# Kernel tuning notes

Hardware: AMD Instinct MI355X
Metric: run time of the kernel (lower is better)

The kernel has to match this reference:

```python
import jax, jax.numpy as jnp
import numpy as np

N_LAYERS = 4
D_MODEL = 256
N_HEADS = 8
D_FF = 2 * D_MODEL
EPS_ATTN = 1e-6
EPS_LN = 1e-5


def setup_inputs() -> dict:
    key = jax.random.key(0)
    ks = jax.random.split(key, 20)
    C, F, L = D_MODEL, D_FF, N_LAYERS
    s = 0.02
    return {
        "ref_feature": jax.random.normal(ks[0], (4, C, 128, 128), jnp.float32),
        # per-layer stacked params (torch nn.Linear convention: y = x @ W.T + b)
        "Wq": jax.random.normal(ks[1], (L, C, C), jnp.float32) * s,
        "bq": jnp.zeros((L, C), jnp.float32),
        "Wk": jax.random.normal(ks[2], (L, C, C), jnp.float32) * s,
        "bk": jnp.zeros((L, C), jnp.float32),
        "Wv": jax.random.normal(ks[3], (L, C, C), jnp.float32) * s,
        "bv": jnp.zeros((L, C), jnp.float32),
        "Wo": jax.random.normal(ks[4], (L, C, C), jnp.float32) * s,
        "bo": jnp.zeros((L, C), jnp.float32),
        "g1": jnp.ones((L, C), jnp.float32),
        "be1": jnp.zeros((L, C), jnp.float32),
        "W1": jax.random.normal(ks[5], (L, F, C), jnp.float32) * s,
        "c1": jnp.zeros((L, F), jnp.float32),
        "W2": jax.random.normal(ks[6], (L, C, F), jnp.float32) * s,
        "c2": jnp.zeros((L, C), jnp.float32),
        "g2": jnp.ones((L, C), jnp.float32),
        "be2": jnp.zeros((L, C), jnp.float32),
    }


def _layer_norm(x, g, b):
    m = jnp.mean(x, axis=-1, keepdims=True)
    v = jnp.mean(jnp.square(x - m), axis=-1, keepdims=True)
    return (x - m) * jax.lax.rsqrt(v + EPS_LN) * g + b


def _feature_map(x):
    return jax.nn.elu(x) + 1.0


def reference(ref_feature, Wq, bq, Wk, bk, Wv, bv, Wo, bo,
              g1, be1, W1, c1, W2, c2, g2, be2):
    N, C, H, W = ref_feature.shape
    Hh, D = N_HEADS, C // N_HEADS
    # patch embed: flatten to tokens [N, HW, C]
    x = ref_feature.reshape(N, C, H * W).transpose(0, 2, 1)

    def body(x, p):
        (Wq_, bq_, Wk_, bk_, Wv_, bv_, Wo_, bo_,
         g1_, be1_, W1_, c1_, W2_, c2_, g2_, be2_) = p
        L = x.shape[1]
        q = (x @ Wq_.T + bq_).reshape(N, L, Hh, D)
        k = (x @ Wk_.T + bk_).reshape(N, L, Hh, D)
        v = (x @ Wv_.T + bv_).reshape(N, L, Hh, D)
        Q = _feature_map(q)
        K = _feature_map(k)
        KV = jnp.einsum('nshd,nshm->nhmd', K, v)            # [N,H,D,D]
        Z = 1.0 / (jnp.einsum('nlhd,nhd->nlh', Q, K.sum(axis=1)) + EPS_ATTN)
        attn = jnp.einsum('nlhd,nhmd,nlh->nlhm', Q, KV, Z).reshape(N, L, C)
        x = _layer_norm(x + attn @ Wo_.T + bo_, g1_, be1_)
        y = jax.nn.relu(x @ W1_.T + c1_) @ W2_.T + c2_
        x = _layer_norm(x + y, g2_, be2_)
        return x, x

    params = (Wq, bq, Wk, bk, Wv, bv, Wo, bo,
              g1, be1, W1, c1, W2, c2, g2, be2)
    _, ys = jax.lax.scan(body, x, params)
    # ys: [n_layers, N, HW, C] -> [n_layers, N, C, H, W]
    return ys.transpose(0, 1, 3, 2).reshape(N_LAYERS, N, C, H, W)
```

## Files before the change

### kernel.cpp

```cpp
#include <hip/hip_runtime.h>
#include <hip/hip_bf16.h>
#include <math.h>

#define NB     4
#define CDIM   256
#define HWDIM  16384
#define LTOK   16384
#define NH     8
#define HD     32
#define FF     512
#define MTOK   (NB * LTOK)
#define NLAYER 4

typedef __bf16 bf16x8 __attribute__((ext_vector_type(8)));
typedef __bf16 bf16x4 __attribute__((ext_vector_type(4)));
typedef float  floatx4 __attribute__((ext_vector_type(4)));

#define GLD16(gp, lp)                                                        \
    __builtin_amdgcn_global_load_lds(                                        \
        (const __attribute__((address_space(1))) void*)(gp),                 \
        (__attribute__((address_space(3))) void*)(lp), 16, 0, 0)

__global__ __launch_bounds__(256)
void f2b_kernel(const float* __restrict__ in, __bf16* __restrict__ out)
{
    int i = (blockIdx.x * 256 + threadIdx.x) * 4;
    float4 f = *(const float4*)&in[i];
    bf16x4 h;
    h[0] = (__bf16)f.x; h[1] = (__bf16)f.y; h[2] = (__bf16)f.z; h[3] = (__bf16)f.w;
    *(bf16x4*)&out[i] = h;
}

__global__ __launch_bounds__(256)
void patch_embed(const float* __restrict__ in, __bf16* __restrict__ out)
{
    __shared__ float tile[32][33];
    const int n = blockIdx.z;
    const int hw0 = blockIdx.x * 32, c0 = blockIdx.y * 32;
    const int tx = threadIdx.x, ty = threadIdx.y;
#pragma unroll
    for (int i = 0; i < 32; i += 8)
        tile[ty + i][tx] = in[(long long)n * CDIM * HWDIM + (long long)(c0 + ty + i) * HWDIM + hw0 + tx];
    __syncthreads();
#pragma unroll
    for (int i = 0; i < 32; i += 8)
        out[(long long)(n * HWDIM + hw0 + ty + i) * CDIM + c0 + tx] = (__bf16)tile[tx][ty + i];
}

__global__ __launch_bounds__(256)
void out_transpose(const __bf16* __restrict__ X, float* __restrict__ out)
{
    __shared__ float tile[32][33];
    const int n = blockIdx.z;
    const int c0 = blockIdx.x * 32, l0 = blockIdx.y * 32;
    const int tid = threadIdx.x;
    {
        int row = tid >> 3, cq = tid & 7;
        bf16x4 x4 = *(const bf16x4*)&X[(long long)(n * LTOK + l0 + row) * CDIM + c0 + cq * 4];
#pragma unroll
        for (int j = 0; j < 4; ++j)
            tile[row][cq * 4 + j] = (float)x4[j];
    }
    __syncthreads();
    {
        int r = tid >> 3, lg = tid & 7;
        float4 o;
        o.x = tile[lg * 4 + 0][r];
        o.y = tile[lg * 4 + 1][r];
        o.z = tile[lg * 4 + 2][r];
        o.w = tile[lg * 4 + 3][r];
        *(float4*)&out[(long long)n * CDIM * LTOK + (long long)(c0 + r) * LTOK + l0 + lg * 4] = o;
    }
}

#define WIDE_PROLOGUE()                                                      \
    const int tid  = threadIdx.x;                                            \
    const int lane = tid & 63;                                               \
    const int wave = tid >> 6;                                               \
    const int m0   = blockIdx.x * 128;                                       \
    const int l15  = lane & 15;                                              \
    const int quad = lane >> 4;                                              \
    const int wm   = (wave & 1) * 64;                                        \
    const int wn   = (wave >> 1) * 128;                                      \
    floatx4 acc[4][8];                                                       \
    _Pragma("unroll")                                                        \
    for (int i = 0; i < 4; ++i)                                              \
        _Pragma("unroll")                                                    \
        for (int j = 0; j < 8; ++j)                                          \
            acc[i][j] = (floatx4){0.f, 0.f, 0.f, 0.f};

#define WIDE_STAGE(Aq, Bq, KD)                                               \
    __syncthreads();                                                         \
    _Pragma("unroll")                                                        \
    for (int i = 0; i < 4; ++i) {                                            \
        int s = wave * 256 + i * 64 + lane;                                  \
        int row = s >> 3, kq = s & 7;                                        \
        GLD16(&(Aq)[(long long)(m0 + row) * (KD) + k0 + kq * 8],             \
              &Asl[(wave * 256 + i * 64) * 8]);                              \
    }                                                                        \
    _Pragma("unroll")                                                        \
    for (int i = 0; i < 8; ++i) {                                            \
        int s = wave * 512 + i * 64 + lane;                                  \
        int row = s >> 3, kq = s & 7;                                        \
        GLD16(&(Bq)[(long long)row * (KD) + k0 + kq * 8],                    \
              &Bsl[(wave * 512 + i * 64) * 8]);                              \
    }                                                                        \
    __syncthreads();

#define WIDE_MFMA()                                                          \
    _Pragma("unroll")                                                        \
    for (int ko = 0; ko < 2; ++ko) {                                         \
        bf16x8 af[4], bfr[8];                                                \
        _Pragma("unroll")                                                    \
        for (int mt = 0; mt < 4; ++mt)                                       \
            af[mt] = *(const bf16x8*)&Asl[(wm + mt * 16 + l15) * 64 + ko * 32 + quad * 8]; \
        _Pragma("unroll")                                                    \
        for (int nt = 0; nt < 8; ++nt)                                       \
            bfr[nt] = *(const bf16x8*)&Bsl[(wn + nt * 16 + l15) * 64 + ko * 32 + quad * 8]; \
        _Pragma("unroll")                                                    \
        for (int mt = 0; mt < 4; ++mt)                                       \
            _Pragma("unroll")                                                \
            for (int nt = 0; nt < 8; ++nt)                                   \
                acc[mt][nt] = __builtin_amdgcn_mfma_f32_16x16x32_bf16(       \
                    bfr[nt], af[mt], acc[mt][nt], 0, 0, 0);                  \
    }

__global__ __launch_bounds__(256, 2)
void gemm_qkv(const __bf16* __restrict__ X,
              const __bf16* __restrict__ Wq, const __bf16* __restrict__ Wk,
              const __bf16* __restrict__ Wv,
              const float* __restrict__ bq, const float* __restrict__ bk,
              const float* __restrict__ bv,
              __bf16* __restrict__ Qo, __bf16* __restrict__ Ko,
              __bf16* __restrict__ Vo)
{
    __shared__ __bf16 Asl[128 * 64];
    __shared__ __bf16 Bsl[256 * 64];
    const int sel = blockIdx.y;
    const __bf16* B    = (sel == 0) ? Wq : (sel == 1) ? Wk : Wv;
    const float*  bias = (sel == 0) ? bq : (sel == 1) ? bk : bv;
    __bf16*       C    = (sel == 0) ? Qo : (sel == 1) ? Ko : Vo;
    const bool do_elu  = sel < 2;

    WIDE_PROLOGUE()
    for (int k0 = 0; k0 < CDIM; k0 += 64) {
        WIDE_STAGE(X, B, CDIM)
        WIDE_MFMA()
    }
#pragma unroll
    for (int mt = 0; mt < 4; ++mt) {
        int row = m0 + wm + mt * 16 + l15;
#pragma unroll
        for (int nt = 0; nt < 8; ++nt) {
            int col0 = wn + nt * 16 + quad * 4;
            float4 bb = *(const float4*)&bias[col0];
            bf16x4 o;
#pragma unroll
            for (int r = 0; r < 4; ++r) {
                float v = acc[mt][nt][r] + ((r == 0) ? bb.x : (r == 1) ? bb.y : (r == 2) ? bb.z : bb.w);
                if (do_elu) v = v > 0.f ? v + 1.f : __expf(v);
                o[r] = (__bf16)v;
            }
            *(bf16x4*)&C[(long long)row * CDIM + col0] = o;
        }
    }
}

__global__ __launch_bounds__(256, 2)
void gemm_relu(const __bf16* __restrict__ A, const __bf16* __restrict__ Bw,
               const float* __restrict__ bias, __bf16* __restrict__ C)
{
    __shared__ __bf16 Asl[128 * 64];
    __shared__ __bf16 Bsl[256 * 64];
    const int n_base = blockIdx.y * 256;
    const __bf16* B = Bw + (long long)n_base * CDIM;

    WIDE_PROLOGUE()
    for (int k0 = 0; k0 < CDIM; k0 += 64) {
        WIDE_STAGE(A, B, CDIM)
        WIDE_MFMA()
    }
#pragma unroll
    for (int mt = 0; mt < 4; ++mt) {
        int row = m0 + wm + mt * 16 + l15;
#pragma unroll
        for (int nt = 0; nt < 8; ++nt) {
            int col0 = wn + nt * 16 + quad * 4;
            float4 bb = *(const float4*)&bias[n_base + col0];
            bf16x4 o;
#pragma unroll
            for (int r = 0; r < 4; ++r) {
                float v = acc[mt][nt][r] + ((r == 0) ? bb.x : (r == 1) ? bb.y : (r == 2) ? bb.z : bb.w);
                o[r] = (__bf16)(v > 0.f ? v : 0.f);
            }
            *(bf16x4*)&C[(long long)row * FF + n_base + col0] = o;
        }
    }
}

template <int KDIM>
__global__ __launch_bounds__(256, 2)
void gemm_ln(const __bf16* __restrict__ A, const __bf16* __restrict__ B,
             const float* __restrict__ bias, __bf16* X,
             const float* __restrict__ g, const float* __restrict__ be)
{
    __shared__ __bf16 Asl[128 * 64];
    __shared__ __bf16 Bsl[256 * 64];

    WIDE_PROLOGUE()
    for (int k0 = 0; k0 < KDIM; k0 += 64) {
        WIDE_STAGE(A, B, KDIM)
        WIDE_MFMA()
    }

#pragma unroll
    for (int mt = 0; mt < 4; ++mt) {
        int row = m0 + wm + mt * 16 + l15;
#pragma unroll
        for (int nt = 0; nt < 8; ++nt) {
            int col0 = wn + nt * 16 + quad * 4;
            float4 bb = *(const float4*)&bias[col0];
            bf16x4 xr = *(const bf16x4*)&X[(long long)row * CDIM + col0];
            acc[mt][nt][0] += bb.x + (float)xr[0];
            acc[mt][nt][1] += bb.y + (float)xr[1];
            acc[mt][nt][2] += bb.z + (float)xr[2];
            acc[mt][nt][3] += bb.w + (float)xr[3];
        }
    }

    float psum[4], psq[4];
#pragma unroll
    for (int mt = 0; mt < 4; ++mt) {
        float s = 0.f, q = 0.f;
#pragma unroll
        for (int nt = 0; nt < 8; ++nt)
#pragma unroll
            for (int r = 0; r < 4; ++r) {
                float v = acc[mt][nt][r];
                s += v; q += v * v;
            }
        s += __shfl_xor(s, 16, 64); s += __shfl_xor(s, 32, 64);
        q += __shfl_xor(q, 16, 64); q += __shfl_xor(q, 32, 64);
        psum[mt] = s; psq[mt] = q;
    }

    float* red = (float*)Asl;
    const int half = wave >> 1;
    __syncthreads();
    if (quad == 0) {
#pragma unroll
        for (int mt = 0; mt < 4; ++mt) {
            int rl = wm + mt * 16 + l15;
            red[rl * 4 + half * 2 + 0] = psum[mt];
            red[rl * 4 + half * 2 + 1] = psq[mt];
        }
    }
    __syncthreads();

#pragma unroll
    for (int mt = 0; mt < 4; ++mt) {
        int rl  = wm + mt * 16 + l15;
        float tot = red[rl * 4 + 0] + red[rl * 4 + 2];
        float tsq = red[rl * 4 + 1] + red[rl * 4 + 3];
        float mean = tot * (1.f / 256.f);
        float var  = tsq * (1.f / 256.f) - mean * mean;
        float rstd = rsqrtf(var + 1e-5f);
        int row = m0 + rl;
#pragma unroll
        for (int nt = 0; nt < 8; ++nt) {
            int col0 = wn + nt * 16 + quad * 4;
            float4 gg = *(const float4*)&g[col0];
            float4 ee = *(const float4*)&be[col0];
            bf16x4 o;
            o[0] = (__bf16)((acc[mt][nt][0] - mean) * rstd * gg.x + ee.x);
            o[1] = (__bf16)((acc[mt][nt][1] - mean) * rstd * gg.y + ee.y);
            o[2] = (__bf16)((acc[mt][nt][2] - mean) * rstd * gg.z + ee.z);
            o[3] = (__bf16)((acc[mt][nt][3] - mean) * rstd * gg.w + ee.w);
            *(bf16x4*)&X[(long long)row * CDIM + col0] = o;
        }
    }
}

__global__ __launch_bounds__(256)
void kv_kernel(const __bf16* __restrict__ Kg, const __bf16* __restrict__ Vg,
               float* __restrict__ KV, float* __restrict__ KS)
{
    __shared__ float Ks[64 * 32];
    __shared__ float Vs[64 * 32];
    const int n = blockIdx.z, h = blockIdx.y;
    const int tid = threadIdx.x;
    const int d  = tid & 31;
    const int m4 = tid >> 5;

    float acc[4] = {0.f, 0.f, 0.f, 0.f};
    float ksum = 0.f;

    for (int sub = 0; sub < 8; ++sub) {
        int s0 = blockIdx.x * 512 + sub * 64;
        __syncthreads();
        {
            int e   = tid * 8;
            int tok = e >> 5, dd = e & 31;
            long long gi = (long long)(n * LTOK + s0 + tok) * CDIM + h * HD + dd;
            bf16x8 kk = *(const bf16x8*)&Kg[gi];
            bf16x8 vv = *(const bf16x8*)&Vg[gi];
#pragma unroll
            for (int j = 0; j < 8; ++j) {
                Ks[e + j] = (float)kk[j];
                Vs[e + j] = (float)vv[j];
            }
        }
        __syncthreads();
#pragma unroll 4
        for (int s = 0; s < 64; ++s) {
            float kd = Ks[s * 32 + d];
            if (m4 == 0) ksum += kd;
#pragma unroll
            for (int j = 0; j < 4; ++j)
                acc[j] += Vs[s * 32 + m4 * 4 + j] * kd;
        }
    }
#pragma unroll
    for (int j = 0; j < 4; ++j)
        atomicAdd(&KV[(((n * NH + h) * HD) + (m4 * 4 + j)) * HD + d], acc[j]);
    if (m4 == 0)
        atomicAdd(&KS[(n * NH + h) * HD + d], ksum);
}

__global__ __launch_bounds__(256)
void attn_kernel(const __bf16* __restrict__ Q, const float* __restrict__ KV,
                 const float* __restrict__ KS, __bf16* __restrict__ out)
{
    __shared__ float q_lds[16 * 256];
    const int n = blockIdx.y;
    const int tid = threadIdx.x;
    const int h = tid >> 5;
    const int m = tid & 31;

    float4 kvr[8], ksr[8];
    {
        const float4* kvp = (const float4*)&KV[(((long long)n * NH + h) * HD + m) * HD];
        const float4* ksp = (const float4*)&KS[((long long)n * NH + h) * HD];
#pragma unroll
        for (int i = 0; i < 8; ++i) { kvr[i] = kvp[i]; ksr[i] = ksp[i]; }
    }

    for (int it = 0; it < 4; ++it) {
        int l0 = blockIdx.x * 64 + it * 16;
        __syncthreads();
#pragma unroll
        for (int i = 0; i < 4; ++i) {
            int e = tid * 4 + i * 1024;
            int row = e >> 8, col = e & 255;
            bf16x4 q4 = *(const bf16x4*)&Q[(long long)(n * LTOK + l0 + row) * CDIM + col];
            float4 f;
            f.x = (float)q4[0]; f.y = (float)q4[1]; f.z = (float)q4[2]; f.w = (float)q4[3];
            *(float4*)&q_lds[e] = f;
        }
        __syncthreads();
#pragma unroll 2
        for (int t = 0; t < 16; ++t) {
            const float4* qr = (const float4*)&q_lds[t * 256 + h * 32];
            float num = 0.f, den = 0.f;
#pragma unroll
            for (int i = 0; i < 8; ++i) {
                float4 q4 = qr[i];
                num += q4.x * kvr[i].x + q4.y * kvr[i].y + q4.z * kvr[i].z + q4.w * kvr[i].w;
                den += q4.x * ksr[i].x + q4.y * ksr[i].y + q4.z * ksr[i].z + q4.w * ksr[i].w;
            }
            out[(long long)(n * LTOK + l0 + t) * CDIM + tid] = (__bf16)(num / (den + 1e-6f));
        }
    }
}

extern "C" void kernel_launch(void* const* d_in, const int* in_sizes, int n_in,
                              void* d_out, int out_size, void* d_ws, size_t ws_size,
                              hipStream_t stream)
{
    const float* ref = (const float*)d_in[0];
    const float* Wq  = (const float*)d_in[1];  const float* bq = (const float*)d_in[2];
    const float* Wk  = (const float*)d_in[3];  const float* bk = (const float*)d_in[4];
    const float* Wv  = (const float*)d_in[5];  const float* bv = (const float*)d_in[6];
    const float* Wo  = (const float*)d_in[7];  const float* bo = (const float*)d_in[8];
    const float* g1  = (const float*)d_in[9];  const float* be1 = (const float*)d_in[10];
    const float* W1  = (const float*)d_in[11]; const float* c1 = (const float*)d_in[12];
    const float* W2  = (const float*)d_in[13]; const float* c2 = (const float*)d_in[14];
    const float* g2  = (const float*)d_in[15]; const float* be2 = (const float*)d_in[16];
    float* out = (float*)d_out;

    const size_t SZ = (size_t)MTOK * CDIM;
    __bf16* Xb = (__bf16*)d_ws;
    __bf16* Qb = Xb + SZ;
    __bf16* Kb = Qb + SZ;
    __bf16* Vb = Kb + SZ;
    __bf16* Hb = Vb + SZ;
    float*  KVb = (float*)(Hb + 2 * SZ);
    float*  KSb = KVb + NB * NH * HD * HD;
    __bf16* Wqb = (__bf16*)(KSb + NB * NH * HD);
    const size_t WC = (size_t)NLAYER * CDIM * CDIM;
    const size_t WF = (size_t)NLAYER * FF * CDIM;
    __bf16* Wkb = Wqb + WC;
    __bf16* Wvb = Wkb + WC;
    __bf16* Wob = Wvb + WC;
    __bf16* W1b = Wob + WC;
    __bf16* W2b = W1b + WF;

    f2b_kernel<<<WC / 1024, 256, 0, stream>>>(Wq, Wqb);
    f2b_kernel<<<WC / 1024, 256, 0, stream>>>(Wk, Wkb);
    f2b_kernel<<<WC / 1024, 256, 0, stream>>>(Wv, Wvb);
    f2b_kernel<<<WC / 1024, 256, 0, stream>>>(Wo, Wob);
    f2b_kernel<<<WF / 1024, 256, 0, stream>>>(W1, W1b);
    f2b_kernel<<<WF / 1024, 256, 0, stream>>>(W2, W2b);

    dim3 tb(32, 8);
    patch_embed<<<dim3(HWDIM / 32, CDIM / 32, NB), tb, 0, stream>>>(ref, Xb);

    for (int l = 0; l < NLAYER; ++l) {
        const __bf16* Wq_l = Wqb + (size_t)l * CDIM * CDIM;
        const __bf16* Wk_l = Wkb + (size_t)l * CDIM * CDIM;
        const __bf16* Wv_l = Wvb + (size_t)l * CDIM * CDIM;
        const __bf16* Wo_l = Wob + (size_t)l * CDIM * CDIM;
        const __bf16* W1_l = W1b + (size_t)l * FF * CDIM;
        const __bf16* W2_l = W2b + (size_t)l * CDIM * FF;
        const float* bq_l = bq + (size_t)l * CDIM;
        const float* bk_l = bk + (size_t)l * CDIM;
        const float* bv_l = bv + (size_t)l * CDIM;
        const float* bo_l = bo + (size_t)l * CDIM;
        const float* c1_l = c1 + (size_t)l * FF;
        const float* c2_l = c2 + (size_t)l * CDIM;
        const float* g1_l = g1 + (size_t)l * CDIM;
        const float* g2_l = g2 + (size_t)l * CDIM;
        const float* be1_l = be1 + (size_t)l * CDIM;
        const float* be2_l = be2 + (size_t)l * CDIM;

        gemm_qkv<<<dim3(MTOK / 128, 3), 256, 0, stream>>>(
            Xb, Wq_l, Wk_l, Wv_l, bq_l, bk_l, bv_l, Qb, Kb, Vb);

        hipMemsetAsync(KVb, 0, (NB * NH * HD * HD + NB * NH * HD) * sizeof(float), stream);
        kv_kernel<<<dim3(LTOK / 512, NH, NB), 256, 0, stream>>>(Kb, Vb, KVb, KSb);

        attn_kernel<<<dim3(LTOK / 64, NB), 256, 0, stream>>>(Qb, KVb, KSb, Kb);

        gemm_ln<CDIM><<<MTOK / 128, 256, 0, stream>>>(Kb, Wo_l, bo_l, Xb, g1_l, be1_l);

        gemm_relu<<<dim3(MTOK / 128, 2), 256, 0, stream>>>(Xb, W1_l, c1_l, Hb);

        gemm_ln<FF><<<MTOK / 128, 256, 0, stream>>>(Hb, W2_l, c2_l, Xb, g2_l, be2_l);

        out_transpose<<<dim3(CDIM / 32, LTOK / 32, NB), 256, 0, stream>>>(
            Xb, out + (size_t)l * NB * CDIM * LTOK);
    }
}
```

Baseline: 1.443 ms.

## Fuse QKV projection with per-tile KV accumulation and add separate reduction kernel

The QKV GEMM now computes Q, K and V for a 64-token tile in one block. K and V stay on chip instead of being written to global memory. Each block transposes K and V into LDS and computes per-head partial K^T V products with MFMA, plus the K column sums. It writes these partials into the now-unused K/V buffers, and a new kv_reduce kernel sums them. This removes the global round trip of K and V, the atomics and the memset. In exchange the GEMM tile is smaller, weights are reloaded three times per block, and an extra reduction pass is added.

```diff
diff --git a/kernel.cpp b/kernel.cpp
--- a/kernel.cpp
+++ b/kernel.cpp
@@ -125,44 +125,210 @@
                     bfr[nt], af[mt], acc[mt][nt], 0, 0, 0);                  \
     }
 
+__device__ __forceinline__ int t_idx(int c, int s)
+{
+    return c * 64 + (s ^ ((c & 7) << 3));
+}
+
 __global__ __launch_bounds__(256, 2)
-void gemm_qkv(const __bf16* __restrict__ X,
-              const __bf16* __restrict__ Wq, const __bf16* __restrict__ Wk,
-              const __bf16* __restrict__ Wv,
-              const float* __restrict__ bq, const float* __restrict__ bk,
-              const float* __restrict__ bv,
-              __bf16* __restrict__ Qo, __bf16* __restrict__ Ko,
-              __bf16* __restrict__ Vo)
-{
-    __shared__ __bf16 Asl[128 * 64];
+void qkv_kv(const __bf16* __restrict__ X,
+            const __bf16* __restrict__ Wq, const __bf16* __restrict__ Wk,
+            const __bf16* __restrict__ Wv,
+            const float* __restrict__ bq, const float* __restrict__ bk,
+            const float* __restrict__ bv,
+            __bf16* __restrict__ Qo, float* __restrict__ pKV,
+            float* __restrict__ pKS)
+{
+    __shared__ __bf16 Asl[64 * 256];
     __shared__ __bf16 Bsl[256 * 64];
-    const int sel = blockIdx.y;
-    const __bf16* B    = (sel == 0) ? Wq : (sel == 1) ? Wk : Wv;
-    const float*  bias = (sel == 0) ? bq : (sel == 1) ? bk : bv;
-    __bf16*       C    = (sel == 0) ? Qo : (sel == 1) ? Ko : Vo;
-    const bool do_elu  = sel < 2;
-
-    WIDE_PROLOGUE()
-    for (int k0 = 0; k0 < CDIM; k0 += 64) {
-        WIDE_STAGE(X, B, CDIM)
-        WIDE_MFMA()
-    }
-#pragma unroll
-    for (int mt = 0; mt < 4; ++mt) {
-        int row = m0 + wm + mt * 16 + l15;
+    const int tid  = threadIdx.x;
+    const int lane = tid & 63;
+    const int wave = tid >> 6;
+    const int m0   = blockIdx.x * 64;
+    const int l15  = lane & 15;
+    const int quad = lane >> 4;
+    const int wm   = (wave & 1) * 32;
+    const int wn   = (wave >> 1) * 128;
+
+#pragma unroll
+    for (int i = 0; i < 8; ++i) {
+        int s = i * 256 + wave * 64 + lane;
+        int row = s >> 5, kq = s & 31;
+        GLD16(&X[(long long)(m0 + row) * CDIM + kq * 8], &Asl[(i * 256 + wave * 64) * 8]);
+    }
+
+    floatx4 acc[2][8];
+    bf16x4  kbf[2][8];
+
+#pragma unroll
+    for (int sel = 0; sel < 3; ++sel) {
+        const __bf16* B = (sel == 0) ? Wq : (sel == 1) ? Wk : Wv;
+#pragma unroll
+        for (int i = 0; i < 2; ++i)
+#pragma unroll
+            for (int j = 0; j < 8; ++j)
+                acc[i][j] = (floatx4){0.f, 0.f, 0.f, 0.f};
+
+        for (int k0 = 0; k0 < CDIM; k0 += 64) {
+            __syncthreads();
+#pragma unroll
+            for (int i = 0; i < 8; ++i) {
+                int s = wave * 512 + i * 64 + lane;
+                int row = s >> 3, kq = s & 7;
+                GLD16(&B[(long long)row * CDIM + k0 + kq * 8], &Bsl[(wave * 512 + i * 64) * 8]);
+            }
+            __syncthreads();
+#pragma unroll
+            for (int ko = 0; ko < 2; ++ko) {
+                bf16x8 af[2], bfr[8];
+#pragma unroll
+                for (int mt = 0; mt < 2; ++mt)
+                    af[mt] = *(const bf16x8*)&Asl[(wm + mt * 16 + l15) * 256 + k0 + ko * 32 + quad * 8];
+#pragma unroll
+                for (int nt = 0; nt < 8; ++nt)
+                    bfr[nt] = *(const bf16x8*)&Bsl[(wn + nt * 16 + l15) * 64 + ko * 32 + quad * 8];
+#pragma unroll
+                for (int mt = 0; mt < 2; ++mt)
+#pragma unroll
+                    for (int nt = 0; nt < 8; ++nt)
+                        acc[mt][nt] = __builtin_amdgcn_mfma_f32_16x16x32_bf16(
+                            bfr[nt], af[mt], acc[mt][nt], 0, 0, 0);
+            }
+        }
+
+        if (sel == 0) {
+#pragma unroll
+            for (int mt = 0; mt < 2; ++mt) {
+                int row = m0 + wm + mt * 16 + l15;
+#pragma unroll
+                for (int nt = 0; nt < 8; ++nt) {
+                    int col0 = wn + nt * 16 + quad * 4;
+                    float4 bb = *(const float4*)&bq[col0];
+                    bf16x4 o;
+#pragma unroll
+                    for (int r = 0; r < 4; ++r) {
+                        float v = acc[mt][nt][r] + ((r == 0) ? bb.x : (r == 1) ? bb.y : (r == 2) ? bb.z : bb.w);
+                        v = v > 0.f ? v + 1.f : __expf(v);
+                        o[r] = (__bf16)v;
+                    }
+                    *(bf16x4*)&Qo[(long long)row * CDIM + col0] = o;
+                }
+            }
+        } else if (sel == 1) {
+#pragma unroll
+            for (int mt = 0; mt < 2; ++mt)
+#pragma unroll
+                for (int nt = 0; nt < 8; ++nt) {
+                    int col0 = wn + nt * 16 + quad * 4;
+                    float4 bb = *(const float4*)&bk[col0];
+#pragma unroll
+                    for (int r = 0; r < 4; ++r) {
+                        float v = acc[mt][nt][r] + ((r == 0) ? bb.x : (r == 1) ? bb.y : (r == 2) ? bb.z : bb.w);
+                        v = v > 0.f ? v + 1.f : __expf(v);
+                        kbf[mt][nt][r] = (__bf16)v;
+                    }
+                }
+        }
+    }
+
+    __syncthreads();
+    {
+        __bf16* KT = Bsl;
+        __bf16* VT = Asl;
 #pragma unroll
         for (int nt = 0; nt < 8; ++nt) {
             int col0 = wn + nt * 16 + quad * 4;
-            float4 bb = *(const float4*)&bias[col0];
-            bf16x4 o;
-#pragma unroll
-            for (int r = 0; r < 4; ++r) {
-                float v = acc[mt][nt][r] + ((r == 0) ? bb.x : (r == 1) ? bb.y : (r == 2) ? bb.z : bb.w);
-                if (do_elu) v = v > 0.f ? v + 1.f : __expf(v);
-                o[r] = (__bf16)v;
-            }
-            *(bf16x4*)&C[(long long)row * CDIM + col0] = o;
-        }
+            float4 bb = *(const float4*)&bv[col0];
+#pragma unroll
+            for (int mt = 0; mt < 2; ++mt) {
+                int row_t = wm + mt * 16 + l15;
+#pragma unroll
+                for (int r = 0; r < 4; ++r) {
+                    KT[t_idx(col0 + r, row_t)] = kbf[mt][nt][r];
+                    float vv = acc[mt][nt][r] + ((r == 0) ? bb.x : (r == 1) ? bb.y : (r == 2) ? bb.z : bb.w);
+                    VT[t_idx(col0 + r, row_t)] = (__bf16)vv;
+                }
+            }
+        }
+    }
+    __syncthreads();
+
+    {
+        const __bf16* KT = Bsl;
+        float s = 0.f;
+#pragma unroll 8
+        for (int i = 0; i < 64; ++i) {
+            int ss = (i + tid) & 63;
+            s += (float)KT[t_idx(tid, ss)];
+        }
+        pKS[(long long)blockIdx.x * 256 + tid] = s;
+    }
+
+    {
+        const __bf16* KT = Bsl;
+        const __bf16* VT = Asl;
+        float* outKV = pKV + (long long)blockIdx.x * 8192;
+#pragma unroll
+        for (int hh = 0; hh < 2; ++hh) {
+            int h = wave * 2 + hh;
+            floatx4 kv[2][2];
+#pragma unroll
+            for (int mi = 0; mi < 2; ++mi)
+#pragma unroll
+                for (int di = 0; di < 2; ++di)
+                    kv[mi][di] = (floatx4){0.f, 0.f, 0.f, 0.f};
+#pragma unroll
+            for (int ks = 0; ks < 2; ++ks) {
+                bf16x8 a[2], b[2];
+#pragma unroll
+                for (int mi = 0; mi < 2; ++mi)
+                    a[mi] = *(const bf16x8*)&VT[t_idx(h * 32 + mi * 16 + l15, ks * 32 + quad * 8)];
+#pragma unroll
+                for (int di = 0; di < 2; ++di)
+                    b[di] = *(const bf16x8*)&KT[t_idx(h * 32 + di * 16 + l15, ks * 32 + quad * 8)];
+#pragma unroll
+                for (int mi = 0; mi < 2; ++mi)
+#pragma unroll
+                    for (int di = 0; di < 2; ++di)
+                        kv[mi][di] = __builtin_amdgcn_mfma_f32_16x16x32_bf16(
+                            a[mi], b[di], kv[mi][di], 0, 0, 0);
+            }
+#pragma unroll
+            for (int mi = 0; mi < 2; ++mi)
+#pragma unroll
+                for (int di = 0; di < 2; ++di)
+#pragma unroll
+                    for (int r = 0; r < 4; ++r)
+                        outKV[(long long)h * 1024 + (mi * 16 + quad * 4 + r) * 32 + di * 16 + l15]
+                            = kv[mi][di][r];
+        }
+    }
+}
+
+__global__ __launch_bounds__(256)
+void kv_reduce(const float* __restrict__ pKV, const float* __restrict__ pKS,
+               float* __restrict__ KV, float* __restrict__ KS)
+{
+    __shared__ float red[256];
+    const int bid = blockIdx.x, tid = threadIdx.x;
+    if (bid < 256) {
+        int o = bid * 128 + (tid & 127);
+        int half = tid >> 7;
+        int n = o >> 13, r = o & 8191;
+        const float* p = pKV + ((long long)n * 256 + half * 128) * 8192 + r;
+        float s = 0.f;
+#pragma unroll 8
+        for (int b = 0; b < 128; ++b) s += p[(long long)b * 8192];
+        red[tid] = s;
+        __syncthreads();
+        if (half == 0) KV[o] = red[tid] + red[tid + 128];
+    } else {
+        int n = bid - 256;
+        const float* p = pKS + (long long)n * 256 * 256 + tid;
+        float s = 0.f;
+#pragma unroll 8
+        for (int b = 0; b < 256; ++b) s += p[b * 256];
+        KS[n * 256 + tid] = s;
     }
 }
 
@@ -279,52 +445,6 @@
             *(bf16x4*)&X[(long long)row * CDIM + col0] = o;
         }
     }
-}
-
-__global__ __launch_bounds__(256)
-void kv_kernel(const __bf16* __restrict__ Kg, const __bf16* __restrict__ Vg,
-               float* __restrict__ KV, float* __restrict__ KS)
-{
-    __shared__ float Ks[64 * 32];
-    __shared__ float Vs[64 * 32];
-    const int n = blockIdx.z, h = blockIdx.y;
-    const int tid = threadIdx.x;
-    const int d  = tid & 31;
-    const int m4 = tid >> 5;
-
-    float acc[4] = {0.f, 0.f, 0.f, 0.f};
-    float ksum = 0.f;
-
-    for (int sub = 0; sub < 8; ++sub) {
-        int s0 = blockIdx.x * 512 + sub * 64;
-        __syncthreads();
-        {
-            int e   = tid * 8;
-            int tok = e >> 5, dd = e & 31;
-            long long gi = (long long)(n * LTOK + s0 + tok) * CDIM + h * HD + dd;
-            bf16x8 kk = *(const bf16x8*)&Kg[gi];
-            bf16x8 vv = *(const bf16x8*)&Vg[gi];
-#pragma unroll
-            for (int j = 0; j < 8; ++j) {
-                Ks[e + j] = (float)kk[j];
-                Vs[e + j] = (float)vv[j];
-            }
-        }
-        __syncthreads();
-#pragma unroll 4
-        for (int s = 0; s < 64; ++s) {
-            float kd = Ks[s * 32 + d];
-            if (m4 == 0) ksum += kd;
-#pragma unroll
-            for (int j = 0; j < 4; ++j)
-                acc[j] += Vs[s * 32 + m4 * 4 + j] * kd;
-        }
-    }
-#pragma unroll
-    for (int j = 0; j < 4; ++j)
-        atomicAdd(&KV[(((n * NH + h) * HD) + (m4 * 4 + j)) * HD + d], acc[j]);
-    if (m4 == 0)
-        atomicAdd(&KS[(n * NH + h) * HD + d], ksum);
 }
 
 __global__ __launch_bounds__(256)
@@ -433,11 +553,11 @@
         const float* be1_l = be1 + (size_t)l * CDIM;
         const float* be2_l = be2 + (size_t)l * CDIM;
 
-        gemm_qkv<<<dim3(MTOK / 128, 3), 256, 0, stream>>>(
-            Xb, Wq_l, Wk_l, Wv_l, bq_l, bk_l, bv_l, Qb, Kb, Vb);
-
-        hipMemsetAsync(KVb, 0, (NB * NH * HD * HD + NB * NH * HD) * sizeof(float), stream);
-        kv_kernel<<<dim3(LTOK / 512, NH, NB), 256, 0, stream>>>(Kb, Vb, KVb, KSb);
+        qkv_kv<<<MTOK / 64, 256, 0, stream>>>(
+            Xb, Wq_l, Wk_l, Wv_l, bq_l, bk_l, bv_l,
+            Qb, (float*)Kb, (float*)Vb);
+
+        kv_reduce<<<260, 256, 0, stream>>>((const float*)Kb, (const float*)Vb, KVb, KSb);
 
         attn_kernel<<<dim3(LTOK / 64, NB), 256, 0, stream>>>(Qb, KVb, KSb, Kb);
 
```

After: 1.398 ms. 1.03x faster.
